# Performance work log

Measured on AMD Instinct MI355X. Metric: run time of the kernel, lower is better.

Reference implementation:

```python
import jax, jax.numpy as jnp
import numpy as np

B, U, N, D, O = 64, 8, 2048, 512, 512  # batch, units, neurons, input_dim, output_dim
RES_CONN, IN_CONN, BIAS_P = 0.2, 0.2, 0.5


def setup_inputs() -> dict:
    key = jax.random.key(0)
    ks = jax.random.split(key, 10)
    # Recurrent weights: normal * sparse mask, normalized by ~spectral radius
    Wd = jax.random.normal(ks[0], (U, N, N), dtype=jnp.float32)
    Wmask = (jax.random.uniform(ks[1], (U, N, N)) < RES_CONN).astype(jnp.float32)
    W = Wd * Wmask / jnp.sqrt(RES_CONN * N)  # approx unit spectral radius
    # Input weights: fixed_bernoulli -> {0,1} sparse matrix
    Win = (jax.random.uniform(ks[2], (U, D, N)) < IN_CONN).astype(jnp.float32)
    bias = (jax.random.uniform(ks[3], (U, 1, N)) < BIAS_P).astype(jnp.float32)
    Wout = jax.random.normal(ks[4], (U, N, O), dtype=jnp.float32)
    sr = jax.random.uniform(ks[5], (U, 1, 1), dtype=jnp.float32)
    adaptive_lr = jax.random.uniform(ks[6], (U, D, 1), dtype=jnp.float32)
    temperature = jnp.ones((1,), dtype=jnp.float32)
    X = jax.random.normal(ks[7], (B, U, D), dtype=jnp.float32)
    state = jax.random.normal(ks[8], (B, U, N), dtype=jnp.float32)
    return {"X": X, "state": state, "W": W, "Win": Win, "bias": bias,
            "Wout": Wout, "sr": sr, "adaptive_lr": adaptive_lr,
            "temperature": temperature}


def reference(X, state, W, Win, bias, Wout, sr, adaptive_lr, temperature):
    # X: [B,U,D], state: [B,U,N]
    x = X[:, :, None, :]       # [B,U,1,D]
    s = state[:, :, None, :]   # [B,U,1,N]
    # adaptive learning rate: softmax over units
    logits = jnp.einsum('buid,udk->buik', x, adaptive_lr) / temperature  # [B,U,1,1]
    lr = jax.nn.softmax(logits, axis=1)
    # _sparse_mm_subhead == masked matmul (W's zeros contribute nothing)
    feed = jnp.einsum('bud,udn->bun', X, Win)[:, :, None, :]           # [B,U,1,N]
    echo = jnp.einsum('bun,unm->bum', state, W * sr)[:, :, None, :] + bias
    new_state = (1.0 - lr) * s + lr * jnp.tanh(feed + echo)            # [B,U,1,N]
    output = jnp.einsum('buin,uno->buio', new_state, Wout)             # [B,U,1,O]
    return new_state.squeeze(2), output.squeeze(2)
```

## Files before the change

kernel.cpp:

```cpp
#include <hip/hip_runtime.h>

#define B_ 64
#define U_ 8
#define N_ 2048
#define D_ 512
#define O_ 512
#define NS_ELEMS ((long)B_ * U_ * N_)
#define OUT_ELEMS ((long)B_ * U_ * O_)

typedef __attribute__((ext_vector_type(8))) short short8;
typedef __attribute__((ext_vector_type(8))) float float8;
typedef __attribute__((ext_vector_type(4))) float float4v;
typedef __attribute__((ext_vector_type(4))) unsigned short ushort4v;
typedef __attribute__((ext_vector_type(16))) float floatx16;

__device__ __forceinline__ float bf2f(unsigned short b) {
    unsigned int u = ((unsigned int)b) << 16;
    float f; __builtin_memcpy(&f, &u, 4); return f;
}
__device__ __forceinline__ unsigned short f2bf(float f) {
    unsigned int u; __builtin_memcpy(&u, &f, 4);
    u += 0x7FFFu + ((u >> 16) & 1u);
    return (unsigned short)(u >> 16);
}
__device__ __forceinline__ bool is_bf(const void* temp) {
    return ((const unsigned short*)temp)[0] == 0x3F80u;
}
__device__ __forceinline__ float ldg1(const void* p, long i, bool bf) {
    return bf ? bf2f(((const unsigned short*)p)[i]) : ((const float*)p)[i];
}
__device__ __forceinline__ short8 ld8(const void* p, long i, bool bf) {
    if (bf) return *(const short8*)((const unsigned short*)p + i);
    float8 v = *(const float8*)((const float*)p + i);
    short8 r;
#pragma unroll
    for (int e = 0; e < 8; ++e) r[e] = (short)f2bf(v[e]);
    return r;
}
__device__ __forceinline__ short8 ld8s(const void* p, long i, bool bf, float s) {
    short8 r;
    if (bf) {
        short8 v = *(const short8*)((const unsigned short*)p + i);
#pragma unroll
        for (int e = 0; e < 8; ++e) r[e] = (short)f2bf(bf2f((unsigned short)v[e]) * s);
    } else {
        float8 v = *(const float8*)((const float*)p + i);
#pragma unroll
        for (int e = 0; e < 8; ++e) r[e] = (short)f2bf(v[e] * s);
    }
    return r;
}
__device__ __forceinline__ void stg1(void* p, long i, bool bf, float v) {
    if (bf) ((unsigned short*)p)[i] = f2bf(v); else ((float*)p)[i] = v;
}
__device__ __forceinline__ int swz(int row, int kbyte) {
    return row * 128 + (kbyte ^ ((row & 7) << 4));
}

__device__ __forceinline__ void gl_lds16(const void* g, void* l) {
    __builtin_amdgcn_global_load_lds(
        (const __attribute__((address_space(1))) unsigned int*)g,
        (__attribute__((address_space(3))) unsigned int*)l, 16, 0, 0);
}
#define WAITV(n) asm volatile("s_waitcnt vmcnt(" #n ")" ::: "memory")

template<bool BF, int NCH>
__device__ __forceinline__ void gemm_wide(
        const char* __restrict__ Apan, long arow_b,
        const char* __restrict__ Bpan, long brow_b,
        char* __restrict__ As,
        char* __restrict__ Bs,
        floatx16& acc0, floatx16& acc1, int t) {
    const int w = t >> 6, l = t & 63;
    const int mrow = (w >> 1) * 32 + (l & 31);
    const int nc0 = (w & 1) * 64 + (l & 31);
    const int BCH = BF ? 16384 : 32768;
    const int a_r = w * 16 + (l >> 3);
    const long a_g = 16 * ((l & 7) ^ (l >> 3));

#define ISSUE2(ck)                                                                  \
    {   char* Ad = As + ((ck) & 1) * 8192 + w * 2048;                               \
        const char* Ag0 = Apan + (long)(ck) * 128;                                  \
        gl_lds16(Ag0 + (long)a_r * arow_b + a_g, Ad);                               \
        gl_lds16(Ag0 + (long)(a_r + 8) * arow_b + a_g, Ad + 1024);                  \
        char* Bd = Bs + ((ck) & 1) * BCH;                                           \
        if (BF) {                                                                   \
            _Pragma("unroll")                                                       \
            for (int i = 0; i < 4; ++i) {                                           \
                int kr = (ck) * 64 + w * 16 + i * 4 + (l >> 4);                     \
                gl_lds16(Bpan + (long)kr * brow_b + (l & 15) * 16,                  \
                         Bd + (w * 16 + i * 4) * 256);                              \
            }                                                                       \
        } else {                                                                    \
            _Pragma("unroll")                                                       \
            for (int i = 0; i < 8; ++i) {                                           \
                int kr = (ck) * 64 + w * 16 + i * 2 + (l >> 5);                     \
                gl_lds16(Bpan + (long)kr * brow_b + (l & 31) * 16,                  \
                         Bd + (w * 16 + i * 2) * 512);                              \
            }                                                                       \
        } }

    ISSUE2(0);
#pragma unroll
    for (int ck = 0; ck < NCH; ++ck) {
        if (ck + 1 < NCH) ISSUE2(ck + 1);
        __builtin_amdgcn_sched_barrier(0);
        if (ck + 1 < NCH) { if (BF) { WAITV(6); } else { WAITV(10); } }
        else { WAITV(0); }
        __builtin_amdgcn_s_barrier();
        __builtin_amdgcn_sched_barrier(0);
        const char* Ac = As + (ck & 1) * 8192;
        const char* Bc = Bs + (ck & 1) * BCH;
#pragma unroll
        for (int ks = 0; ks < 4; ++ks) {
            int g = 2 * ks + (l >> 5);
            short8 a = *(const short8*)(Ac + swz(mrow, g * 16));
            short8 b0, b1;
            if (BF) {
#pragma unroll
                for (int e = 0; e < 8; ++e) {
                    b0[e] = *(const short*)(Bc + (g * 8 + e) * 256 + nc0 * 2);
                    b1[e] = *(const short*)(Bc + (g * 8 + e) * 256 + (nc0 + 32) * 2);
                }
            } else {
#pragma unroll
                for (int e = 0; e < 8; ++e) {
                    b0[e] = (short)f2bf(*(const float*)(Bc + (g * 8 + e) * 512 + nc0 * 4));
                    b1[e] = (short)f2bf(*(const float*)(Bc + (g * 8 + e) * 512 + (nc0 + 32) * 4));
                }
            }
            acc0 = __builtin_amdgcn_mfma_f32_32x32x16_bf16(a, b0, acc0, 0, 0, 0);
            acc1 = __builtin_amdgcn_mfma_f32_32x32x16_bf16(a, b1, acc1, 0, 0, 0);
        }
        __builtin_amdgcn_sched_barrier(0);
        __builtin_amdgcn_s_barrier();
    }
#undef ISSUE2
}

__global__ __launch_bounds__(256) void k01(
        const void* __restrict__ state, const void* __restrict__ X,
        const void* __restrict__ sr, const void* __restrict__ alr,
        const void* __restrict__ temp,
        unsigned short* __restrict__ stC, unsigned short* __restrict__ xC,
        float* __restrict__ lrbuf) {
    const bool bf = is_bf(temp);
    const int bid = blockIdx.x;
    const int t = threadIdx.x;
    __shared__ float lg[U_];
    if (bid < 1280) {
        const long i = ((long)bid * 256 + t) * 4;
        ushort4v o;
        if (i < NS_ELEMS) {
            const int u = (int)(i >> 17);
            const float srv = ldg1(sr, u, bf);
#pragma unroll
            for (int e = 0; e < 4; ++e) {
                const long j = i + e;
                const int b = (int)((j >> 11) & 63), k = (int)(j & 2047);
                o[e] = f2bf(ldg1(state, (long)(b * 8 + u) * 2048 + k, bf) * srv);
            }
            *(ushort4v*)(stC + i) = o;
        } else {
            const long j0 = i - NS_ELEMS;
            const int u = (int)(j0 >> 15);
#pragma unroll
            for (int e = 0; e < 4; ++e) {
                const long j = j0 + e;
                const int b = (int)((j >> 9) & 63), k = (int)(j & 511);
                o[e] = f2bf(ldg1(X, (long)(b * 8 + u) * 512 + k, bf));
            }
            *(ushort4v*)(xC + j0) = o;
        }
    } else {
        const int b = bid - 1280;
        const int u = t >> 5, ln = t & 31;
        float s = 0.f;
#pragma unroll
        for (int j = 0; j < 16; ++j) {
            int d = ln * 16 + j;
            s += ldg1(X, (long)(b * 8 + u) * 512 + d, bf) * ldg1(alr, u * 512 + d, bf);
        }
#pragma unroll
        for (int off = 1; off < 32; off <<= 1) s += __shfl_xor(s, off);
        const float T = ldg1(temp, 0, bf);
        if (ln == 0) lg[u] = s / T;
        __syncthreads();
        if (t < U_) {
            float m = lg[0];
#pragma unroll
            for (int i = 1; i < U_; ++i) m = fmaxf(m, lg[i]);
            float den = 0.f;
#pragma unroll
            for (int i = 0; i < U_; ++i) den += expf(lg[i] - m);
            lrbuf[b * U_ + t] = expf(lg[t] - m) / den;
        }
    }
}

template<bool BF>
__device__ __forceinline__ void k2w_body(
        const unsigned short* stC, const unsigned short* xC,
        const void* W, const void* Win, unsigned short* slabs,
        char* As, char* Bs, int bid, int t) {
    const int seg = bid >> 7;
    const int u   = (bid >> 4) & 7;
    const int nb  = bid & 15;
    const int n0  = nb * 128;
    const int w = t >> 6, l = t & 63;
    const long esz = BF ? 2 : 4;
    floatx16 acc0, acc1;
#pragma unroll
    for (int i = 0; i < 16; ++i) { acc0[i] = 0.f; acc1[i] = 0.f; }

    const char* stP = (const char*)stC + (long)u * 262144;
    const char* Wp  = (const char*)W + ((long)u * N_ * N_ + n0) * esz;

    if (seg == 0) {
        gemm_wide<BF, 8>((const char*)xC + (long)u * 65536, 1024,
                         (const char*)Win + ((long)u * D_ * N_ + n0) * esz, N_ * esz,
                         As, Bs, acc0, acc1, t);
        gemm_wide<BF, 2>(stP, 4096, Wp, N_ * esz, As, Bs, acc0, acc1, t);
    } else if (seg == 1) {
        gemm_wide<BF, 10>(stP + 256, 4096, Wp + (long)128 * N_ * esz, N_ * esz,
                          As, Bs, acc0, acc1, t);
    } else if (seg == 2) {
        gemm_wide<BF, 10>(stP + 1536, 4096, Wp + (long)768 * N_ * esz, N_ * esz,
                          As, Bs, acc0, acc1, t);
    } else {
        gemm_wide<BF, 10>(stP + 2816, 4096, Wp + (long)1408 * N_ * esz, N_ * esz,
                          As, Bs, acc0, acc1, t);
    }
    unsigned short* slab = slabs + (long)seg * NS_ELEMS;
    const int n = n0 + (w & 1) * 64 + (l & 31);
    const int rowbase = (w >> 1) * 32 + 4 * (l >> 5);
#pragma unroll
    for (int r = 0; r < 16; ++r) {
        int b = rowbase + (r & 3) + 8 * (r >> 2);
        slab[(long)b * (U_ * N_) + u * N_ + n] = f2bf(acc0[r]);
        slab[(long)b * (U_ * N_) + u * N_ + n + 32] = f2bf(acc1[r]);
    }
}

__global__ __launch_bounds__(256) void k2_wide(
        const unsigned short* __restrict__ stC, const unsigned short* __restrict__ xC,
        const void* __restrict__ W, const void* __restrict__ Win,
        const void* __restrict__ temp, unsigned short* __restrict__ slabs) {
    __shared__ alignas(16) char As[2 * 8192];
    __shared__ alignas(16) char Bs[2 * 32768];
    const int bid = (blockIdx.x % 8) * 64 + blockIdx.x / 8;
    if (is_bf(temp))
        k2w_body<true >(stC, xC, W, Win, slabs, As, Bs, bid, threadIdx.x);
    else
        k2w_body<false>(stC, xC, W, Win, slabs, As, Bs, bid, threadIdx.x);
}

__global__ void k2b_mix(const unsigned short* __restrict__ slabs,
                        const void* __restrict__ state,
                        const void* __restrict__ bias, const void* __restrict__ temp,
                        const float* __restrict__ lrbuf, void* __restrict__ ns,
                        unsigned short* __restrict__ nsC) {
    const bool bf = is_bf(temp);
    const long i = ((long)blockIdx.x * 256 + threadIdx.x) * 4;
    const int b = (int)(i >> 14);
    const int un = (int)(i & 16383);
    const int u = un >> 11, n = un & 2047;
    float4v s;
    {
        ushort4v v0 = *(const ushort4v*)(slabs + i);
        ushort4v v1 = *(const ushort4v*)(slabs + NS_ELEMS + i);
        ushort4v v2 = *(const ushort4v*)(slabs + 2 * NS_ELEMS + i);
        ushort4v v3 = *(const ushort4v*)(slabs + 3 * NS_ELEMS + i);
#pragma unroll
        for (int e = 0; e < 4; ++e)
            s[e] = (bf2f(v0[e]) + bf2f(v1[e])) + (bf2f(v2[e]) + bf2f(v3[e]));
    }
    const float lr = lrbuf[b * U_ + u];
    ushort4v oc;
#pragma unroll
    for (int e = 0; e < 4; ++e) {
        float st = ldg1(state, i + e, bf);
        float bv = ldg1(bias, u * N_ + n + e, bf);
        float v = (1.f - lr) * st + lr * tanhf(s[e] + bv);
        stg1(ns, i + e, bf, v);
        oc[e] = f2bf(v);
    }
    *(ushort4v*)(nsC + ((long)u * 64 + b) * 2048 + n) = oc;
}

template<bool BF>
__device__ __forceinline__ void k3w_body(
        const unsigned short* nsC, const void* Wout, unsigned short* part,
        char* As, char* Bs, int bid, int t) {
    const int kc = bid >> 5;
    const int u  = (bid >> 2) & 7;
    const int ot = bid & 3;
    const int o0 = ot * 128;
    const int w = t >> 6, l = t & 63;
    const long esz = BF ? 2 : 4;
    floatx16 acc0, acc1;
#pragma unroll
    for (int i = 0; i < 16; ++i) { acc0[i] = 0.f; acc1[i] = 0.f; }
    gemm_wide<BF, 2>((const char*)nsC + (long)u * 262144 + (long)kc * 256, 4096,
                     (const char*)Wout + ((long)u * N_ * O_ + (long)kc * 128 * O_ + o0) * esz,
                     O_ * esz, As, Bs, acc0, acc1, t);
    unsigned short* slab = part + (long)((kc * 8 + u) * 4 + ot) * 8192;
    const int oo = (w & 1) * 64 + (l & 31);
    const int rowbase = (w >> 1) * 32 + 4 * (l >> 5);
#pragma unroll
    for (int r = 0; r < 16; ++r) {
        int b = rowbase + (r & 3) + 8 * (r >> 2);
        slab[b * 128 + oo] = f2bf(acc0[r]);
        slab[b * 128 + oo + 32] = f2bf(acc1[r]);
    }
}

__global__ __launch_bounds__(256) void k3_wide(
        const unsigned short* __restrict__ nsC, const void* __restrict__ Wout,
        const void* __restrict__ temp, unsigned short* __restrict__ part) {
    __shared__ alignas(16) char As[2 * 8192];
    __shared__ alignas(16) char Bs[2 * 32768];
    const int bid = (blockIdx.x % 8) * 64 + blockIdx.x / 8;
    if (is_bf(temp))
        k3w_body<true >(nsC, Wout, part, As, Bs, bid, threadIdx.x);
    else
        k3w_body<false>(nsC, Wout, part, As, Bs, bid, threadIdx.x);
}

__global__ void k3_reduce(const unsigned short* __restrict__ part,
                          const void* __restrict__ temp,
                          void* __restrict__ outfull) {
    const bool bf = is_bf(temp);
    int i = blockIdx.x * 256 + threadIdx.x;
    int b = i >> 12;
    int u = (i >> 9) & 7;
    int o = i & 511;
    int ot = o >> 7, oo = o & 127;
    float s = 0.f;
#pragma unroll
    for (int kc = 0; kc < 16; ++kc)
        s += bf2f(part[(long)((kc * 8 + u) * 4 + ot) * 8192 + b * 128 + oo]);
    stg1(outfull, NS_ELEMS + i, bf, s);
}

__global__ __launch_bounds__(256) void k2_state(
        const void* __restrict__ X, const void* __restrict__ state,
        const void* __restrict__ W, const void* __restrict__ Win,
        const void* __restrict__ bias, const void* __restrict__ sr,
        const void* __restrict__ temp, const float* __restrict__ lrbuf,
        void* __restrict__ ns) {
    const bool bf = is_bf(temp);
    const int u  = blockIdx.x >> 5;
    const int n0 = (blockIdx.x & 31) * 64;
    const int t = threadIdx.x;
    const int w = t >> 6, l = t & 63;
    __shared__ alignas(16) char As[8192];
    __shared__ alignas(16) char Bs[8192];
    const float srv = ldg1(sr, u, bf);
    floatx16 acc;
#pragma unroll
    for (int i = 0; i < 16; ++i) acc[i] = 0.f;
    for (int ck = 0; ck < 40; ++ck) {
        const bool feed = ck < 8;
        const void* Ag; long aoff; int lda; float ascale;
        const void* Bg; long boff;
        if (feed) {
            Ag = X;   aoff = (long)u * D_ + ck * 64;          lda = U_ * D_; ascale = 1.f;
            Bg = Win; boff = (long)u * D_ * N_ + (long)(ck * 64) * N_ + n0;
        } else {
            Ag = state; aoff = (long)u * N_ + (ck - 8) * 64;  lda = U_ * N_; ascale = srv;
            Bg = W;     boff = (long)u * N_ * N_ + (long)((ck - 8) * 64) * N_ + n0;
        }
        __syncthreads();
#pragma unroll
        for (int j = 0; j < 2; ++j) {
            int idx = j * 256 + t;
            int row = idx >> 3, cch = idx & 7;
            short8 v = ld8s(Ag, aoff + (long)row * lda + cch * 8, bf, ascale);
            *(short8*)(As + swz(row, cch * 16)) = v;
        }
#pragma unroll
        for (int j = 0; j < 2; ++j) {
            int k = t & 63;
            int c = (t >> 6) + 4 * j;
            short8 v = ld8(Bg, boff + (long)k * N_ + c * 8, bf);
#pragma unroll
            for (int e = 0; e < 8; ++e) {
                int n = c * 8 + e;
                *(unsigned short*)(Bs + swz(n, 2 * k)) = (unsigned short)v[e];
            }
        }
        __syncthreads();
        const int mrow = (w >> 1) * 32 + (l & 31);
        const int ncol = (w & 1) * 32 + (l & 31);
#pragma unroll
        for (int ks = 0; ks < 4; ++ks) {
            int g = 2 * ks + (l >> 5);
            short8 a = *(const short8*)(As + swz(mrow, g * 16));
            short8 b = *(const short8*)(Bs + swz(ncol, g * 16));
            acc = __builtin_amdgcn_mfma_f32_32x32x16_bf16(a, b, acc, 0, 0, 0);
        }
    }
    const int n = n0 + (w & 1) * 32 + (l & 31);
    const int rowbase = (w >> 1) * 32 + 4 * (l >> 5);
    const float biasv = ldg1(bias, u * N_ + n, bf);
#pragma unroll
    for (int r = 0; r < 16; ++r) {
        int b = rowbase + (r & 3) + 8 * (r >> 2);
        float lr = lrbuf[b * U_ + u];
        float st = ldg1(state, (long)b * U_ * N_ + u * N_ + n, bf);
        float v = (1.f - lr) * st + lr * tanhf(acc[r] + biasv);
        stg1(ns, (long)b * U_ * N_ + u * N_ + n, bf, v);
    }
}

__global__ __launch_bounds__(256) void k3_mono(
        const void* __restrict__ ns, const void* __restrict__ Wout,
        const void* __restrict__ temp, void* __restrict__ outfull) {
    const bool bf = is_bf(temp);
    const int u  = (blockIdx.x >> 3) & 7;
    const int ot = blockIdx.x & 7;
    const int o0 = ot * 64;
    const int t = threadIdx.x;
    const int w = t >> 6, l = t & 63;
    __shared__ alignas(16) char As[8192];
    __shared__ alignas(16) char Bs[8192];
    floatx16 acc;
#pragma unroll
    for (int i = 0; i < 16; ++i) acc[i] = 0.f;
    for (int ck = 0; ck < 32; ++ck) {
        const long ka = (long)(ck * 64);
        __syncthreads();
#pragma unroll
        for (int j = 0; j < 2; ++j) {
            int idx = j * 256 + t;
            int row = idx >> 3, cch = idx & 7;
            short8 v = ld8(ns, (long)row * (U_ * N_) + u * N_ + ka + cch * 8, bf);
            *(short8*)(As + swz(row, cch * 16)) = v;
        }
#pragma unroll
        for (int j = 0; j < 2; ++j) {
            int k = t & 63;
            int c = (t >> 6) + 4 * j;
            short8 v = ld8(Wout, (long)u * N_ * O_ + (ka + k) * O_ + o0 + c * 8, bf);
#pragma unroll
            for (int e = 0; e < 8; ++e) {
                int n = c * 8 + e;
                *(unsigned short*)(Bs + swz(n, 2 * k)) = (unsigned short)v[e];
            }
        }
        __syncthreads();
        const int mrow = (w >> 1) * 32 + (l & 31);
        const int ncol = (w & 1) * 32 + (l & 31);
#pragma unroll
        for (int ks = 0; ks < 4; ++ks) {
            int g = 2 * ks + (l >> 5);
            short8 a = *(const short8*)(As + swz(mrow, g * 16));
            short8 b = *(const short8*)(Bs + swz(ncol, g * 16));
            acc = __builtin_amdgcn_mfma_f32_32x32x16_bf16(a, b, acc, 0, 0, 0);
        }
    }
    const int oo = (w & 1) * 32 + (l & 31);
    const int rowbase = (w >> 1) * 32 + 4 * (l >> 5);
#pragma unroll
    for (int r = 0; r < 16; ++r) {
        int b = rowbase + (r & 3) + 8 * (r >> 2);
        stg1(outfull, NS_ELEMS + (long)b * U_ * O_ + u * O_ + o0 + oo, bf, acc[r]);
    }
}

extern "C" void kernel_launch(void* const* d_in, const int* in_sizes, int n_in,
                              void* d_out, int out_size, void* d_ws, size_t ws_size,
                              hipStream_t stream) {
    const void* X     = d_in[0];
    const void* state = d_in[1];
    const void* W     = d_in[2];
    const void* Win   = d_in[3];
    const void* bias  = d_in[4];
    const void* Wout  = d_in[5];
    const void* sr    = d_in[6];
    const void* alr   = d_in[7];
    const void* temp  = d_in[8];

    char* base = (char*)d_ws;
    float* lrbuf        = (float*)base;
    unsigned short* stC = (unsigned short*)(base + 4096);
    unsigned short* xC  = (unsigned short*)(base + 4096 + (2u << 20));
    unsigned short* nsC = (unsigned short*)(base + 4096 + (2u << 20) + (512u << 10));
    unsigned short* slabs = (unsigned short*)(base + (8u << 20));
    const size_t need = (8u << 20) + 4 * (size_t)NS_ELEMS * 2;

    if (ws_size >= need) {
        k01      <<<1344, 256, 0, stream>>>(state, X, sr, alr, temp, stC, xC, lrbuf);
        k2_wide  <<<512, 256, 0, stream>>>(stC, xC, W, Win, temp, slabs);
        k2b_mix  <<<NS_ELEMS / 1024, 256, 0, stream>>>(slabs, state, bias, temp, lrbuf, d_out, nsC);
        k3_wide  <<<512, 256, 0, stream>>>(nsC, Wout, temp, slabs);
        k3_reduce<<<OUT_ELEMS / 256, 256, 0, stream>>>(slabs, temp, d_out);
    } else {
        k01      <<<1344, 256, 0, stream>>>(state, X, sr, alr, temp,
                                            (unsigned short*)base, (unsigned short*)base, lrbuf);
        k2_state <<<256, 256, 0, stream>>>(X, state, W, Win, bias, sr, temp, lrbuf, d_out);
        k3_mono  <<<64, 256, 0, stream>>>(d_out, Wout, temp, d_out);
    }
}
```

Before: 59.63 us.

## Fuse state-mix epilogue into output GEMM prologue, drop separate mix kernel

Measured after the change: 84.50 us. +41.7%, slower.

```diff
diff --git a/kernel.cpp b/kernel.cpp
--- a/kernel.cpp
+++ b/kernel.cpp
@@ -9,6 +9,7 @@
 #define OUT_ELEMS ((long)B_ * U_ * O_)
 
 typedef __attribute__((ext_vector_type(8))) short short8;
+typedef __attribute__((ext_vector_type(8))) unsigned short ushort8;
 typedef __attribute__((ext_vector_type(8))) float float8;
 typedef __attribute__((ext_vector_type(4))) float float4v;
 typedef __attribute__((ext_vector_type(4))) unsigned short ushort4v;
@@ -55,6 +56,9 @@
 }
 __device__ __forceinline__ int swz(int row, int kbyte) {
     return row * 128 + (kbyte ^ ((row & 7) << 4));
+}
+__device__ __forceinline__ int swz256(int row, int kbyte) {
+    return row * 256 + (kbyte ^ ((row & 15) << 4));
 }
 
 __device__ __forceinline__ void gl_lds16(const void* g, void* l) {
@@ -255,55 +259,113 @@
         k2w_body<false>(stC, xC, W, Win, slabs, As, Bs, bid, threadIdx.x);
 }
 
-__global__ void k2b_mix(const unsigned short* __restrict__ slabs,
-                        const void* __restrict__ state,
-                        const void* __restrict__ bias, const void* __restrict__ temp,
-                        const float* __restrict__ lrbuf, void* __restrict__ ns,
-                        unsigned short* __restrict__ nsC) {
-    const bool bf = is_bf(temp);
-    const long i = ((long)blockIdx.x * 256 + threadIdx.x) * 4;
-    const int b = (int)(i >> 14);
-    const int un = (int)(i & 16383);
-    const int u = un >> 11, n = un & 2047;
-    float4v s;
-    {
-        ushort4v v0 = *(const ushort4v*)(slabs + i);
-        ushort4v v1 = *(const ushort4v*)(slabs + NS_ELEMS + i);
-        ushort4v v2 = *(const ushort4v*)(slabs + 2 * NS_ELEMS + i);
-        ushort4v v3 = *(const ushort4v*)(slabs + 3 * NS_ELEMS + i);
-#pragma unroll
-        for (int e = 0; e < 4; ++e)
-            s[e] = (bf2f(v0[e]) + bf2f(v1[e])) + (bf2f(v2[e]) + bf2f(v3[e]));
-    }
-    const float lr = lrbuf[b * U_ + u];
-    ushort4v oc;
-#pragma unroll
-    for (int e = 0; e < 4; ++e) {
-        float st = ldg1(state, i + e, bf);
-        float bv = ldg1(bias, u * N_ + n + e, bf);
-        float v = (1.f - lr) * st + lr * tanhf(s[e] + bv);
-        stg1(ns, i + e, bf, v);
-        oc[e] = f2bf(v);
-    }
-    *(ushort4v*)(nsC + ((long)u * 64 + b) * 2048 + n) = oc;
-}
-
 template<bool BF>
-__device__ __forceinline__ void k3w_body(
-        const unsigned short* nsC, const void* Wout, unsigned short* part,
-        char* As, char* Bs, int bid, int t) {
+__device__ __forceinline__ void k3f_body(
+        const unsigned short* slabs, const void* state, const void* bias,
+        const float* lrbuf, const void* Wout, void* ns,
+        unsigned short* part, char* As, char* Bs, int bid, int t) {
     const int kc = bid >> 5;
     const int u  = (bid >> 2) & 7;
     const int ot = bid & 3;
     const int o0 = ot * 128;
     const int w = t >> 6, l = t & 63;
     const long esz = BF ? 2 : 4;
+    const int BCH = BF ? 16384 : 32768;
+    const char* Bpan = (const char*)Wout + ((long)u * N_ * O_ + (long)kc * 128 * O_ + o0) * esz;
+    const long brow_b = O_ * esz;
+
+#define ISSUE_B(ck)                                                                 \
+    {   char* Bd = Bs + ((ck) & 1) * BCH;                                           \
+        if (BF) {                                                                   \
+            _Pragma("unroll")                                                       \
+            for (int i = 0; i < 4; ++i) {                                           \
+                int kr = (ck) * 64 + w * 16 + i * 4 + (l >> 4);                     \
+                gl_lds16(Bpan + (long)kr * brow_b + (l & 15) * 16,                  \
+                         Bd + (w * 16 + i * 4) * 256);                              \
+            }                                                                       \
+        } else {                                                                    \
+            _Pragma("unroll")                                                       \
+            for (int i = 0; i < 8; ++i) {                                           \
+                int kr = (ck) * 64 + w * 16 + i * 2 + (l >> 5);                     \
+                gl_lds16(Bpan + (long)kr * brow_b + (l & 31) * 16,                  \
+                         Bd + (w * 16 + i * 2) * 512);                              \
+            }                                                                       \
+        } }
+
+    ISSUE_B(0);
+    __builtin_amdgcn_sched_barrier(0);
+
+    {
+        const int br = t >> 2, q = t & 3;
+        const long nbase = (long)kc * 128 + q * 32;
+        const long rowoff = ((long)br * 8 + u) * 2048;
+        const float lr = lrbuf[br * 8 + u];
+#pragma unroll
+        for (int j = 0; j < 4; ++j) {
+            const long idx = rowoff + nbase + j * 8;
+            ushort8 v0 = *(const ushort8*)(slabs + idx);
+            ushort8 v1 = *(const ushort8*)(slabs + NS_ELEMS + idx);
+            ushort8 v2 = *(const ushort8*)(slabs + 2 * NS_ELEMS + idx);
+            ushort8 v3 = *(const ushort8*)(slabs + 3 * NS_ELEMS + idx);
+            short8 ov;
+#pragma unroll
+            for (int e = 0; e < 8; ++e) {
+                float s = (bf2f(v0[e]) + bf2f(v1[e])) + (bf2f(v2[e]) + bf2f(v3[e]));
+                float st = ldg1(state, idx + e, BF);
+                float bv = ldg1(bias, (long)u * 2048 + nbase + j * 8 + e, BF);
+                float v = (1.f - lr) * st + lr * tanhf(s + bv);
+                if (ot == 0) stg1(ns, idx + e, BF, v);
+                ov[e] = (short)f2bf(v);
+            }
+            *(short8*)(As + swz256(br, (int)(2 * (q * 32 + j * 8)))) = ov;
+        }
+    }
+    asm volatile("s_waitcnt lgkmcnt(0)" ::: "memory");
+    __builtin_amdgcn_s_barrier();
+    __builtin_amdgcn_sched_barrier(0);
+
+    const int mrow = (w >> 1) * 32 + (l & 31);
+    const int nc0 = (w & 1) * 64 + (l & 31);
     floatx16 acc0, acc1;
 #pragma unroll
     for (int i = 0; i < 16; ++i) { acc0[i] = 0.f; acc1[i] = 0.f; }
-    gemm_wide<BF, 2>((const char*)nsC + (long)u * 262144 + (long)kc * 256, 4096,
-                     (const char*)Wout + ((long)u * N_ * O_ + (long)kc * 128 * O_ + o0) * esz,
-                     O_ * esz, As, Bs, acc0, acc1, t);
+#pragma unroll
+    for (int ck = 0; ck < 2; ++ck) {
+        if (ck == 0) {
+            ISSUE_B(1);
+            __builtin_amdgcn_sched_barrier(0);
+            if (BF) { WAITV(4); } else { WAITV(8); }
+        } else {
+            WAITV(0);
+        }
+        __builtin_amdgcn_s_barrier();
+        __builtin_amdgcn_sched_barrier(0);
+        const char* Bc = Bs + (ck & 1) * BCH;
+#pragma unroll
+        for (int ks = 0; ks < 4; ++ks) {
+            int g = 2 * ks + (l >> 5);
+            short8 a = *(const short8*)(As + swz256(mrow, ck * 128 + g * 16));
+            short8 b0, b1;
+            if (BF) {
+#pragma unroll
+                for (int e = 0; e < 8; ++e) {
+                    b0[e] = *(const short*)(Bc + (g * 8 + e) * 256 + nc0 * 2);
+                    b1[e] = *(const short*)(Bc + (g * 8 + e) * 256 + (nc0 + 32) * 2);
+                }
+            } else {
+#pragma unroll
+                for (int e = 0; e < 8; ++e) {
+                    b0[e] = (short)f2bf(*(const float*)(Bc + (g * 8 + e) * 512 + nc0 * 4));
+                    b1[e] = (short)f2bf(*(const float*)(Bc + (g * 8 + e) * 512 + (nc0 + 32) * 4));
+                }
+            }
+            acc0 = __builtin_amdgcn_mfma_f32_32x32x16_bf16(a, b0, acc0, 0, 0, 0);
+            acc1 = __builtin_amdgcn_mfma_f32_32x32x16_bf16(a, b1, acc1, 0, 0, 0);
+        }
+        __builtin_amdgcn_sched_barrier(0);
+        __builtin_amdgcn_s_barrier();
+    }
+#undef ISSUE_B
     unsigned short* slab = part + (long)((kc * 8 + u) * 4 + ot) * 8192;
     const int oo = (w & 1) * 64 + (l & 31);
     const int rowbase = (w >> 1) * 32 + 4 * (l >> 5);
@@ -315,16 +377,18 @@
     }
 }
 
-__global__ __launch_bounds__(256) void k3_wide(
-        const unsigned short* __restrict__ nsC, const void* __restrict__ Wout,
-        const void* __restrict__ temp, unsigned short* __restrict__ part) {
-    __shared__ alignas(16) char As[2 * 8192];
+__global__ __launch_bounds__(256) void k3_fused(
+        const unsigned short* __restrict__ slabs, const void* __restrict__ state,
+        const void* __restrict__ bias, const float* __restrict__ lrbuf,
+        const void* __restrict__ Wout, const void* __restrict__ temp,
+        void* __restrict__ ns, unsigned short* __restrict__ part) {
+    __shared__ alignas(16) char As[16384];
     __shared__ alignas(16) char Bs[2 * 32768];
     const int bid = (blockIdx.x % 8) * 64 + blockIdx.x / 8;
     if (is_bf(temp))
-        k3w_body<true >(nsC, Wout, part, As, Bs, bid, threadIdx.x);
+        k3f_body<true >(slabs, state, bias, lrbuf, Wout, ns, part, As, Bs, bid, threadIdx.x);
     else
-        k3w_body<false>(nsC, Wout, part, As, Bs, bid, threadIdx.x);
+        k3f_body<false>(slabs, state, bias, lrbuf, Wout, ns, part, As, Bs, bid, threadIdx.x);
 }
 
 __global__ void k3_reduce(const unsigned short* __restrict__ part,
@@ -486,16 +550,15 @@
     float* lrbuf        = (float*)base;
     unsigned short* stC = (unsigned short*)(base + 4096);
     unsigned short* xC  = (unsigned short*)(base + 4096 + (2u << 20));
-    unsigned short* nsC = (unsigned short*)(base + 4096 + (2u << 20) + (512u << 10));
     unsigned short* slabs = (unsigned short*)(base + (8u << 20));
-    const size_t need = (8u << 20) + 4 * (size_t)NS_ELEMS * 2;
+    unsigned short* part  = (unsigned short*)(base + (16u << 20));
+    const size_t need = (16u << 20) + 4 * (size_t)NS_ELEMS * 2;
 
     if (ws_size >= need) {
         k01      <<<1344, 256, 0, stream>>>(state, X, sr, alr, temp, stC, xC, lrbuf);
         k2_wide  <<<512, 256, 0, stream>>>(stC, xC, W, Win, temp, slabs);
-        k2b_mix  <<<NS_ELEMS / 1024, 256, 0, stream>>>(slabs, state, bias, temp, lrbuf, d_out, nsC);
-        k3_wide  <<<512, 256, 0, stream>>>(nsC, Wout, temp, slabs);
-        k3_reduce<<<OUT_ELEMS / 256, 256, 0, stream>>>(slabs, temp, d_out);
+        k3_fused <<<512, 256, 0, stream>>>(slabs, state, bias, lrbuf, Wout, temp, d_out, part);
+        k3_reduce<<<OUT_ELEMS / 256, 256, 0, stream>>>(part, temp, d_out);
     } else {
         k01      <<<1344, 256, 0, stream>>>(state, X, sr, alr, temp,
                                             (unsigned short*)base, (unsigned short*)base, lrbuf);
```
